# Performance work log

Measured on AMD Instinct MI355X. Metric: run time of the kernel, lower is better.

Reference implementation:

```python
import jax, jax.numpy as jnp
import numpy as np

N = 170000      # nodes
E = 2400000     # edges
F_IN = 128      # dataset.num_features
H = 64          # hidden_channels
C = 40          # dataset.num_classes
L = 8           # num_layers
ENTROPY = 1.0   # args.entropy
EPS = 1e-20


def setup_inputs() -> dict:
    key = jax.random.key(0)
    ks = jax.random.split(key, 10)
    x = jax.random.normal(ks[0], (N, F_IN), jnp.float32)
    edge_src = jax.random.randint(ks[1], (E,), 0, N)
    edge_dst = jax.random.randint(ks[2], (E,), 0, N)
    edge_weight = jax.random.uniform(ks[3], (E,), jnp.float32) / 14.0  # ~1/deg scale
    u = jax.random.uniform(ks[4], (N, L + 1), jnp.float32, 1e-6, 1.0 - 1e-6)
    gumbel = -jnp.log(-jnp.log(u))  # standard Gumbel noise for gumbel_softmax
    lin0_w = jax.random.normal(ks[5], (F_IN, H), jnp.float32) / np.float32(np.sqrt(F_IN))
    lin0_b = jnp.zeros((H,), jnp.float32)
    meta_w = jax.random.normal(ks[6], (H, 1), jnp.float32) / np.float32(np.sqrt(H))
    meta_b = jnp.zeros((1,), jnp.float32)
    lin1_w = jax.random.normal(ks[7], (H, C), jnp.float32) / np.float32(np.sqrt(H))
    lin1_b = jnp.zeros((C,), jnp.float32)
    return dict(x=x, edge_weight=edge_weight, gumbel=gumbel,
                lin0_w=lin0_w, lin0_b=lin0_b, meta_w=meta_w, meta_b=meta_b,
                lin1_w=lin1_w, lin1_b=lin1_b,
                edge_src=edge_src, edge_dst=edge_dst)


def reference(x, edge_weight, gumbel, lin0_w, lin0_b, meta_w, meta_b,
              lin1_w, lin1_b, edge_src, edge_dst):
    # input projection + relu (dropout=0 -> no-op)
    x = jnp.maximum(x @ lin0_w + lin0_b, 0.0)  # [N,H]
    xs = [x]
    # GCNII layers with conv.alpha = conv.beta = 0 -> pure edge-weighted
    # scatter-add propagation followed by relu.
    for _ in range(L):
        msg = edge_weight[:, None] * x[edge_src]              # [E,H] gather
        x = jax.ops.segment_sum(msg, edge_dst, num_segments=N)  # [N,H] scatter-add
        x = jnp.maximum(x, 0.0)
        xs.append(x)
    xMat = jnp.stack(xs, axis=1)  # [N, L+1, H] (preds == xMatrix since concat='none')
    # MetaNet: [N, L+1]
    r = jnp.squeeze(xMat @ meta_w, -1) + meta_b[0]
    # get_t: stick-breaking with sigmoid; last column uses t=1 times cumprod
    s = jax.nn.sigmoid(r)                                    # [N, L+1]
    cp_excl = jnp.concatenate(
        [jnp.ones((N, 1), s.dtype), jnp.cumprod(1.0 - s, axis=1)[:, :-1]], axis=1)
    t = s * cp_excl
    t = t.at[:, -1].set(cp_excl[:, -1])
    ent_loss = ENTROPY * (-(jnp.log(t + EPS) * t).sum(1).mean())
    # gumbel_softmax(log(t+eps), tau=1, hard=False)
    tM = jax.nn.softmax(jnp.log(t + EPS) + gumbel, axis=1)   # [N, L+1]
    # layer mixing: [N,1,L+1] @ [N,L+1,H] -> [N,H]
    out = jnp.einsum('nl,nlh->nh', tM, xMat)
    out = out @ lin1_w + lin1_b
    return jax.nn.log_softmax(out, axis=-1), ent_loss
```

## Files before the change

kernel.cpp:

```cpp
#include <hip/hip_runtime.h>
#include <hip/hip_bf16.h>

#define N_NODES 170000
#define N_EDGES 2400000
#define F_IN_   128
#define H_      64
#define C_OUT   40
#define L_LAYERS 8
#define LP1     9
#define EPS_T   1e-20f
#define ROW_ELEMS (LP1 * H_)

typedef unsigned short u16;
typedef short bf16x8 __attribute__((ext_vector_type(8)));
typedef float f32x4 __attribute__((ext_vector_type(4)));

__device__ __forceinline__ float bf2f(u16 u) {
    union { unsigned int i; float f; } c; c.i = ((unsigned int)u) << 16; return c.f;
}
__device__ __forceinline__ u16 f2bf(float f) {
    __hip_bfloat16 h = __float2bfloat16(f);
    return *reinterpret_cast<u16*>(&h);
}

__device__ __forceinline__ float waveReduceSum(float v) {
    for (int m = 32; m; m >>= 1) v += __shfl_xor(v, m, 64);
    return v;
}
__device__ __forceinline__ float waveReduceMax(float v) {
    for (int m = 32; m; m >>= 1) v = fmaxf(v, __shfl_xor(v, m, 64));
    return v;
}

__global__ __launch_bounds__(256) void k_zero4(float4* __restrict__ p) {
    p[blockIdx.x * 256 + threadIdx.x] = make_float4(0.f, 0.f, 0.f, 0.f);
}

__global__ __launch_bounds__(256) void k_hist(
    const int* __restrict__ edst, int* __restrict__ deg)
{
    int e = blockIdx.x * 256 + threadIdx.x;
    if (e < N_EDGES) atomicAdd(&deg[edst[e]], 1);
}

#define SCAN_TPB 256
#define SCAN_VPT 8
#define SCAN_EPB (SCAN_TPB * SCAN_VPT)
#define SCAN_BLOCKS ((N_NODES + SCAN_EPB - 1) / SCAN_EPB)

__global__ __launch_bounds__(SCAN_TPB) void k_scan1(
    const int* __restrict__ deg, int* __restrict__ rowstart,
    int* __restrict__ blockSums)
{
    __shared__ int tsum[SCAN_TPB];
    int tid = threadIdx.x;
    int base = blockIdx.x * SCAN_EPB + tid * SCAN_VPT;
    int vals[SCAN_VPT];
    int local = 0;
    #pragma unroll
    for (int i = 0; i < SCAN_VPT; ++i) {
        int idx = base + i;
        int v = (idx < N_NODES) ? deg[idx] : 0;
        vals[i] = local;
        local += v;
    }
    tsum[tid] = local;
    __syncthreads();
    for (int off = 1; off < SCAN_TPB; off <<= 1) {
        int v = (tid >= off) ? tsum[tid - off] : 0;
        __syncthreads();
        tsum[tid] += v;
        __syncthreads();
    }
    int texcl = tsum[tid] - local;
    #pragma unroll
    for (int i = 0; i < SCAN_VPT; ++i) {
        int idx = base + i;
        if (idx < N_NODES) rowstart[idx] = texcl + vals[i];
    }
    if (tid == SCAN_TPB - 1) blockSums[blockIdx.x] = tsum[tid];
}

__global__ __launch_bounds__(64) void k_scan2(int* __restrict__ blockSums) {
    if (threadIdx.x == 0) {
        int acc = 0;
        for (int i = 0; i < SCAN_BLOCKS; ++i) {
            int v = blockSums[i];
            blockSums[i] = acc;
            acc += v;
        }
    }
}

__global__ __launch_bounds__(SCAN_TPB) void k_scan3(
    int* __restrict__ rowstart, const int* __restrict__ blockSums)
{
    int off = blockSums[blockIdx.x];
    int base = blockIdx.x * SCAN_EPB + threadIdx.x * SCAN_VPT;
    #pragma unroll
    for (int i = 0; i < SCAN_VPT; ++i) {
        int idx = base + i;
        if (idx < N_NODES) rowstart[idx] += off;
    }
}

__global__ __launch_bounds__(256) void k_bucket(
    const int* __restrict__ esrc, const int* __restrict__ edst,
    const float* __restrict__ ew, const int* __restrict__ rowstart,
    int* __restrict__ cursor, int2* __restrict__ csr, int lo, int hi)
{
    int e = blockIdx.x * 256 + threadIdx.x;
    if (e >= N_EDGES) return;
    int d = edst[e];
    if (d < lo || d >= hi) return;
    int p = rowstart[d] + atomicAdd(&cursor[d], 1);
    csr[p] = make_int2(esrc[e], __float_as_int(ew[e]));
}

__global__ __launch_bounds__(256) void k_lin0(
    const float* __restrict__ x, const float* __restrict__ W0,
    const float* __restrict__ b0, const float* __restrict__ mw,
    const float* __restrict__ mb, u16* __restrict__ xMatB,
    float* __restrict__ r)
{
    __shared__ u16 Wt[H_ * F_IN_];
    int tid = threadIdx.x;
    for (int i = tid; i < F_IN_ * H_; i += 256) {
        int k = i >> 6, c = i & 63;
        Wt[c * F_IN_ + (k ^ ((c & 7) << 3))] = f2bf(W0[i]);
    }
    __syncthreads();

    int wave = tid >> 6, lane = tid & 63;
    int lg = lane >> 4;
    int lr = lane & 15;

    bf16x8 bfrag[4][4];
    float b0v[4], mwv[4];
    #pragma unroll
    for (int ct = 0; ct < 4; ++ct) {
        int c = ct * 16 + lr;
        #pragma unroll
        for (int kt = 0; kt < 4; ++kt) {
            int kidx = (kt * 32 + lg * 8) ^ ((c & 7) << 3);
            bfrag[ct][kt] = *reinterpret_cast<bf16x8*>(&Wt[c * F_IN_ + kidx]);
        }
        b0v[ct] = b0[c];
        mwv[ct] = mw[c];
    }
    float mb0 = mb[0];

    int nbase = blockIdx.x * 256 + wave * 64;
    #pragma unroll
    for (int m = 0; m < 4; ++m) {
        int arow = nbase + m * 16 + lr;
        int arowc = (arow < N_NODES) ? arow : (N_NODES - 1);
        const float4* xrow = (const float4*)(x + (size_t)arowc * F_IN_);
        f32x4 acc[4];
        #pragma unroll
        for (int ct = 0; ct < 4; ++ct) {
            acc[ct][0] = b0v[ct]; acc[ct][1] = b0v[ct];
            acc[ct][2] = b0v[ct]; acc[ct][3] = b0v[ct];
        }
        #pragma unroll
        for (int kt = 0; kt < 4; ++kt) {
            int k8 = kt * 8 + lg * 2;
            float4 xa = xrow[k8];
            float4 xb = xrow[k8 + 1];
            bf16x8 a;
            a[0] = (short)f2bf(xa.x); a[1] = (short)f2bf(xa.y);
            a[2] = (short)f2bf(xa.z); a[3] = (short)f2bf(xa.w);
            a[4] = (short)f2bf(xb.x); a[5] = (short)f2bf(xb.y);
            a[6] = (short)f2bf(xb.z); a[7] = (short)f2bf(xb.w);
            #pragma unroll
            for (int ct = 0; ct < 4; ++ct)
                acc[ct] = __builtin_amdgcn_mfma_f32_16x16x32_bf16(
                    a, bfrag[ct][kt], acc[ct], 0, 0, 0);
        }
        float p[4];
        #pragma unroll
        for (int reg = 0; reg < 4; ++reg) {
            int n = nbase + m * 16 + lg * 4 + reg;
            float pr = 0.f;
            #pragma unroll
            for (int ct = 0; ct < 4; ++ct) {
                float v = fmaxf(acc[ct][reg], 0.f);
                if (n < N_NODES)
                    xMatB[(size_t)n * ROW_ELEMS + ct * 16 + lr] = f2bf(v);
                pr = fmaf(v, mwv[ct], pr);
            }
            p[reg] = pr;
        }
        #pragma unroll
        for (int reg = 0; reg < 4; ++reg) {
            p[reg] += __shfl_xor(p[reg], 1, 64);
            p[reg] += __shfl_xor(p[reg], 2, 64);
            p[reg] += __shfl_xor(p[reg], 4, 64);
            p[reg] += __shfl_xor(p[reg], 8, 64);
        }
        if (lr < 4) {
            int n = nbase + m * 16 + lg * 4 + lr;
            if (n < N_NODES) r[n * LP1] = p[lr] + mb0;
        }
    }
}

__global__ __launch_bounds__(256) void k_prop(
    const u16* __restrict__ xMatB, int l,
    const int* __restrict__ rowstart, const int* __restrict__ deg,
    const int2* __restrict__ csr,
    const float* __restrict__ mw, const float* __restrict__ mb,
    u16* __restrict__ xMatOut, float* __restrict__ r)
{
    int tid = threadIdx.x, wave = tid >> 6, lane = tid & 63;
    int n = blockIdx.x * 4 + wave;
    int sl = lane & 15, q = lane >> 4;
    int start = rowstart[n];
    int d = deg[n];
    int dm1 = (d > 0) ? (d - 1) : 0;

    int myS = 0; float myW = 0.f;
    if (lane < d) {
        int2 e = csr[start + lane];
        myS = e.x; myW = __int_as_float(e.y);
    }
    const unsigned loff = (unsigned)l * H_ + sl * 4;

    float a0x = 0.f, a0y = 0.f, a0z = 0.f, a0w = 0.f;
    float a1x = 0.f, a1y = 0.f, a1z = 0.f, a1w = 0.f;
    float a2x = 0.f, a2y = 0.f, a2z = 0.f, a2w = 0.f;
    float a3x = 0.f, a3y = 0.f, a3z = 0.f, a3w = 0.f;

    int dmax = (d < 64) ? d : 64;
    int kb = 0;
    do {
        int idx0 = kb + q;
        int idx1 = kb + q + 4;
        int idx2 = kb + q + 8;
        int idx3 = kb + q + 12;
        int ic0 = (idx0 < dm1) ? idx0 : dm1;
        int ic1 = (idx1 < dm1) ? idx1 : dm1;
        int ic2 = (idx2 < dm1) ? idx2 : dm1;
        int ic3 = (idx3 < dm1) ? idx3 : dm1;
        int   s0 = __shfl(myS, ic0, 64); float w0 = __shfl(myW, ic0, 64);
        int   s1 = __shfl(myS, ic1, 64); float w1 = __shfl(myW, ic1, 64);
        int   s2 = __shfl(myS, ic2, 64); float w2 = __shfl(myW, ic2, 64);
        int   s3 = __shfl(myS, ic3, 64); float w3 = __shfl(myW, ic3, 64);
        if (idx0 >= d) w0 = 0.f;
        if (idx1 >= d) w1 = 0.f;
        if (idx2 >= d) w2 = 0.f;
        if (idx3 >= d) w3 = 0.f;
        ushort4 v0 = *reinterpret_cast<const ushort4*>(
            &xMatB[(size_t)(unsigned)s0 * ROW_ELEMS + loff]);
        ushort4 v1 = *reinterpret_cast<const ushort4*>(
            &xMatB[(size_t)(unsigned)s1 * ROW_ELEMS + loff]);
        ushort4 v2 = *reinterpret_cast<const ushort4*>(
            &xMatB[(size_t)(unsigned)s2 * ROW_ELEMS + loff]);
        ushort4 v3 = *reinterpret_cast<const ushort4*>(
            &xMatB[(size_t)(unsigned)s3 * ROW_ELEMS + loff]);
        a0x = fmaf(bf2f(v0.x), w0, a0x); a0y = fmaf(bf2f(v0.y), w0, a0y);
        a0z = fmaf(bf2f(v0.z), w0, a0z); a0w = fmaf(bf2f(v0.w), w0, a0w);
        a1x = fmaf(bf2f(v1.x), w1, a1x); a1y = fmaf(bf2f(v1.y), w1, a1y);
        a1z = fmaf(bf2f(v1.z), w1, a1z); a1w = fmaf(bf2f(v1.w), w1, a1w);
        a2x = fmaf(bf2f(v2.x), w2, a2x); a2y = fmaf(bf2f(v2.y), w2, a2y);
        a2z = fmaf(bf2f(v2.z), w2, a2z); a2w = fmaf(bf2f(v2.w), w2, a2w);
        a3x = fmaf(bf2f(v3.x), w3, a3x); a3y = fmaf(bf2f(v3.y), w3, a3y);
        a3z = fmaf(bf2f(v3.z), w3, a3z); a3w = fmaf(bf2f(v3.w), w3, a3w);
        kb += 16;
    } while (kb < dmax);

    for (int kb2 = 64; kb2 < d; kb2 += 16) {
        #pragma unroll
        for (int j = 0; j < 4; ++j) {
            int idx = kb2 + j * 4 + q;
            if (idx < d) {
                int2 e = csr[start + idx];
                float w = __int_as_float(e.y);
                ushort4 v = *reinterpret_cast<const ushort4*>(
                    &xMatB[(size_t)(unsigned)e.x * ROW_ELEMS + loff]);
                a0x = fmaf(bf2f(v.x), w, a0x);
                a0y = fmaf(bf2f(v.y), w, a0y);
                a0z = fmaf(bf2f(v.z), w, a0z);
                a0w = fmaf(bf2f(v.w), w, a0w);
            }
        }
    }

    float r0 = a0x + a1x + a2x + a3x;
    float r1 = a0y + a1y + a2y + a3y;
    float r2 = a0z + a1z + a2z + a3z;
    float r3 = a0w + a1w + a2w + a3w;
    r0 += __shfl_xor(r0, 16, 64); r0 += __shfl_xor(r0, 32, 64);
    r1 += __shfl_xor(r1, 16, 64); r1 += __shfl_xor(r1, 32, 64);
    r2 += __shfl_xor(r2, 16, 64); r2 += __shfl_xor(r2, 32, 64);
    r3 += __shfl_xor(r3, 16, 64); r3 += __shfl_xor(r3, 32, 64);
    r0 = fmaxf(r0, 0.f); r1 = fmaxf(r1, 0.f);
    r2 = fmaxf(r2, 0.f); r3 = fmaxf(r3, 0.f);
    if (q == 0) {
        ushort4 o; o.x = f2bf(r0); o.y = f2bf(r1); o.z = f2bf(r2); o.w = f2bf(r3);
        *reinterpret_cast<ushort4*>(
            &xMatOut[(size_t)n * ROW_ELEMS + (l + 1) * H_ + sl * 4]) = o;
    }
    float dot = r0 * mw[4 * sl] + r1 * mw[4 * sl + 1] +
                r2 * mw[4 * sl + 2] + r3 * mw[4 * sl + 3];
    dot += __shfl_xor(dot, 1, 64);
    dot += __shfl_xor(dot, 2, 64);
    dot += __shfl_xor(dot, 4, 64);
    dot += __shfl_xor(dot, 8, 64);
    if (lane == 0) r[n * LP1 + (l + 1)] = dot + mb[0];
}

__global__ __launch_bounds__(256) void k_gate(
    const float* __restrict__ r, const float* __restrict__ gum,
    float* __restrict__ tM, float* __restrict__ entPart)
{
    __shared__ float lds[4];
    int tid = threadIdx.x;
    int n = blockIdx.x * 256 + tid;
    float ent = 0.f;
    if (n < N_NODES) {
        float t[LP1], lg[LP1];
        float cp = 1.f;
        #pragma unroll
        for (int j = 0; j < LP1; ++j) {
            float rv = r[n * LP1 + j];
            float s = 1.f / (1.f + expf(-rv));
            t[j] = (j == L_LAYERS) ? cp : s * cp;
            cp *= (1.f - s);
        }
        float mx = -INFINITY;
        #pragma unroll
        for (int j = 0; j < LP1; ++j) {
            float lt = logf(t[j] + EPS_T);
            ent -= t[j] * lt;
            lg[j] = lt + gum[n * LP1 + j];
            mx = fmaxf(mx, lg[j]);
        }
        float se = 0.f;
        #pragma unroll
        for (int j = 0; j < LP1; ++j) { lg[j] = expf(lg[j] - mx); se += lg[j]; }
        float inv = 1.f / se;
        #pragma unroll
        for (int j = 0; j < LP1; ++j) tM[n * LP1 + j] = lg[j] * inv;
    }
    float s = waveReduceSum(ent);
    int wave = tid >> 6, lane = tid & 63;
    if (lane == 0) lds[wave] = s;
    __syncthreads();
    if (tid == 0) entPart[blockIdx.x] = lds[0] + lds[1] + lds[2] + lds[3];
}

__global__ __launch_bounds__(256) void k_final(
    const u16* __restrict__ xMatB, const float* __restrict__ tM,
    const float* __restrict__ W1, const float* __restrict__ b1,
    float* __restrict__ out)
{
    __shared__ float mixLds[4][H_];
    int tid = threadIdx.x, wave = tid >> 6, lane = tid & 63;
    int n = blockIdx.x * 4 + wave;
    float tm = (lane < LP1) ? tM[n * LP1 + lane] : 0.f;
    float m = 0.f;
    #pragma unroll
    for (int j = 0; j < LP1; ++j) {
        float w = __shfl(tm, j, 64);
        m = fmaf(w, bf2f(xMatB[(size_t)n * ROW_ELEMS + j * H_ + lane]), m);
    }
    mixLds[wave][lane] = m;
    __syncthreads();
    float o = -INFINITY;
    if (lane < C_OUT) {
        float a = b1[lane];
        #pragma unroll 8
        for (int h = 0; h < H_; ++h)
            a = fmaf(mixLds[wave][h], W1[h * C_OUT + lane], a);
        o = a;
    }
    float omx = waveReduceMax(o);
    float ex = (lane < C_OUT) ? expf(o - omx) : 0.f;
    float es = waveReduceSum(ex);
    if (lane < C_OUT)
        out[(size_t)n * C_OUT + lane] = o - omx - logf(es);
}

__global__ __launch_bounds__(256) void k_entreduce(
    const float* __restrict__ part, int n, float scale, float* __restrict__ out)
{
    __shared__ float lds[4];
    int tid = threadIdx.x;
    float s = 0.f;
    for (int i = tid; i < n; i += 256) s += part[i];
    s = waveReduceSum(s);
    int wave = tid >> 6, lane = tid & 63;
    if (lane == 0) lds[wave] = s;
    __syncthreads();
    if (tid == 0) out[0] = (lds[0] + lds[1] + lds[2] + lds[3]) * scale;
}

extern "C" void kernel_launch(void* const* d_in, const int* in_sizes, int n_in,
                              void* d_out, int out_size, void* d_ws, size_t ws_size,
                              hipStream_t stream)
{
    const float* x   = (const float*)d_in[0];
    const float* ew  = (const float*)d_in[1];
    const float* gum = (const float*)d_in[2];
    const float* W0  = (const float*)d_in[3];
    const float* b0  = (const float*)d_in[4];
    const float* mw  = (const float*)d_in[5];
    const float* mb  = (const float*)d_in[6];
    const float* W1  = (const float*)d_in[7];
    const float* b1  = (const float*)d_in[8];
    const int* esrc  = (const int*)d_in[9];
    const int* edst  = (const int*)d_in[10];
    float* out = (float*)d_out;

    const size_t xMatBytes = (size_t)N_NODES * ROW_ELEMS * sizeof(u16);
    const size_t rBytes    = (size_t)N_NODES * LP1 * sizeof(float);
    const size_t tMBytes   = (size_t)N_NODES * LP1 * sizeof(float);
    const size_t entBytes  = (size_t)((N_NODES + 255) / 256) * sizeof(float);
    const size_t degBytes  = (size_t)N_NODES * sizeof(int);
    const size_t curBytes  = (size_t)N_NODES * sizeof(int);
    const size_t rowBytes  = (size_t)N_NODES * sizeof(int);
    const size_t bsBytes   = 512;
    const size_t csrBytes  = (size_t)N_EDGES * sizeof(int2);
    const size_t need = xMatBytes + rBytes + tMBytes + entBytes + degBytes +
                        curBytes + rowBytes + bsBytes + csrBytes;
    if (ws_size < need) return;

    char* p = (char*)d_ws;
    u16*  xMatB    = (u16*)p;           p += xMatBytes;
    float* rbuf    = (float*)p;         p += rBytes;
    float* tMbuf   = (float*)p;         p += tMBytes;
    float* entP    = (float*)p;         p += entBytes;
    int*  deg      = (int*)p;           p += degBytes;
    int*  cursor   = (int*)p;           p += curBytes;
    int*  rowstart = (int*)p;           p += rowBytes;
    int*  blockSums= (int*)p;           p += bsBytes;
    int2* csr      = (int2*)p;

    const int nodeBlocks = N_NODES / 4;
    const int edgeBlocks = (N_EDGES + 255) / 256;
    const int gateBlocks = (N_NODES + 255) / 256;
    const int lin0Blocks = (N_NODES + 255) / 256;

    k_zero4<<<333, 256, 0, stream>>>((float4*)deg);
    k_hist<<<edgeBlocks, 256, 0, stream>>>(edst, deg);
    k_scan1<<<SCAN_BLOCKS, SCAN_TPB, 0, stream>>>(deg, rowstart, blockSums);
    k_scan2<<<1, 64, 0, stream>>>(blockSums);
    k_scan3<<<SCAN_BLOCKS, SCAN_TPB, 0, stream>>>(rowstart, blockSums);
    const int STEP = N_NODES / 8;
    for (int i = 0; i < 8; ++i)
        k_bucket<<<edgeBlocks, 256, 0, stream>>>(esrc, edst, ew, rowstart,
                                                 cursor, csr, i * STEP,
                                                 (i + 1) * STEP);

    k_lin0<<<lin0Blocks, 256, 0, stream>>>(x, W0, b0, mw, mb, xMatB, rbuf);
    for (int l = 0; l < L_LAYERS; ++l)
        k_prop<<<nodeBlocks, 256, 0, stream>>>(xMatB, l, rowstart, deg, csr,
                                               mw, mb, xMatB, rbuf);
    k_gate<<<gateBlocks, 256, 0, stream>>>(rbuf, gum, tMbuf, entP);
    k_final<<<nodeBlocks, 256, 0, stream>>>(xMatB, tMbuf, W1, b1, out);
    k_entreduce<<<1, 256, 0, stream>>>(entP, gateBlocks, 1.0f / N_NODES,
                                       out + (size_t)N_NODES * C_OUT);
}
```

Measured before the change: 872.9 us.

## Map eight lanes per node in propagation with 16-byte gathers

Restructures the propagation kernel so each node is handled by 8 lanes instead of a full wave. Each lane gathers 8 bf16 features (16 bytes) per edge and walks the edge list sequentially, two edges at a time. This removes the shuffle-based edge distribution and the cross-quarter reductions, and raises the number of nodes processed per block from 4 to 32. The cost is that the loop runs until the highest-degree node among the wave's 8 nodes is finished, so lanes on shorter rows sit idle, and each lane issues fewer independent loads in flight. Every lane also reloads its own CSR entries, which increases redundant index loads.

```diff
diff --git a/kernel.cpp b/kernel.cpp
--- a/kernel.cpp
+++ b/kernel.cpp
@@ -12,6 +12,7 @@
 #define ROW_ELEMS (LP1 * H_)
 
 typedef unsigned short u16;
+typedef unsigned short u16x8 __attribute__((ext_vector_type(8)));
 typedef short bf16x8 __attribute__((ext_vector_type(8)));
 typedef float f32x4 __attribute__((ext_vector_type(4)));
 
@@ -212,102 +213,56 @@
     const float* __restrict__ mw, const float* __restrict__ mb,
     u16* __restrict__ xMatOut, float* __restrict__ r)
 {
-    int tid = threadIdx.x, wave = tid >> 6, lane = tid & 63;
-    int n = blockIdx.x * 4 + wave;
-    int sl = lane & 15, q = lane >> 4;
-    int start = rowstart[n];
-    int d = deg[n];
-    int dm1 = (d > 0) ? (d - 1) : 0;
-
-    int myS = 0; float myW = 0.f;
-    if (lane < d) {
-        int2 e = csr[start + lane];
-        myS = e.x; myW = __int_as_float(e.y);
-    }
-    const unsigned loff = (unsigned)l * H_ + sl * 4;
-
-    float a0x = 0.f, a0y = 0.f, a0z = 0.f, a0w = 0.f;
-    float a1x = 0.f, a1y = 0.f, a1z = 0.f, a1w = 0.f;
-    float a2x = 0.f, a2y = 0.f, a2z = 0.f, a2w = 0.f;
-    float a3x = 0.f, a3y = 0.f, a3z = 0.f, a3w = 0.f;
-
-    int dmax = (d < 64) ? d : 64;
-    int kb = 0;
-    do {
-        int idx0 = kb + q;
-        int idx1 = kb + q + 4;
-        int idx2 = kb + q + 8;
-        int idx3 = kb + q + 12;
-        int ic0 = (idx0 < dm1) ? idx0 : dm1;
-        int ic1 = (idx1 < dm1) ? idx1 : dm1;
-        int ic2 = (idx2 < dm1) ? idx2 : dm1;
-        int ic3 = (idx3 < dm1) ? idx3 : dm1;
-        int   s0 = __shfl(myS, ic0, 64); float w0 = __shfl(myW, ic0, 64);
-        int   s1 = __shfl(myS, ic1, 64); float w1 = __shfl(myW, ic1, 64);
-        int   s2 = __shfl(myS, ic2, 64); float w2 = __shfl(myW, ic2, 64);
-        int   s3 = __shfl(myS, ic3, 64); float w3 = __shfl(myW, ic3, 64);
-        if (idx0 >= d) w0 = 0.f;
-        if (idx1 >= d) w1 = 0.f;
-        if (idx2 >= d) w2 = 0.f;
-        if (idx3 >= d) w3 = 0.f;
-        ushort4 v0 = *reinterpret_cast<const ushort4*>(
-            &xMatB[(size_t)(unsigned)s0 * ROW_ELEMS + loff]);
-        ushort4 v1 = *reinterpret_cast<const ushort4*>(
-            &xMatB[(size_t)(unsigned)s1 * ROW_ELEMS + loff]);
-        ushort4 v2 = *reinterpret_cast<const ushort4*>(
-            &xMatB[(size_t)(unsigned)s2 * ROW_ELEMS + loff]);
-        ushort4 v3 = *reinterpret_cast<const ushort4*>(
-            &xMatB[(size_t)(unsigned)s3 * ROW_ELEMS + loff]);
-        a0x = fmaf(bf2f(v0.x), w0, a0x); a0y = fmaf(bf2f(v0.y), w0, a0y);
-        a0z = fmaf(bf2f(v0.z), w0, a0z); a0w = fmaf(bf2f(v0.w), w0, a0w);
-        a1x = fmaf(bf2f(v1.x), w1, a1x); a1y = fmaf(bf2f(v1.y), w1, a1y);
-        a1z = fmaf(bf2f(v1.z), w1, a1z); a1w = fmaf(bf2f(v1.w), w1, a1w);
-        a2x = fmaf(bf2f(v2.x), w2, a2x); a2y = fmaf(bf2f(v2.y), w2, a2y);
-        a2z = fmaf(bf2f(v2.z), w2, a2z); a2w = fmaf(bf2f(v2.w), w2, a2w);
-        a3x = fmaf(bf2f(v3.x), w3, a3x); a3y = fmaf(bf2f(v3.y), w3, a3y);
-        a3z = fmaf(bf2f(v3.z), w3, a3z); a3w = fmaf(bf2f(v3.w), w3, a3w);
-        kb += 16;
-    } while (kb < dmax);
-
-    for (int kb2 = 64; kb2 < d; kb2 += 16) {
-        #pragma unroll
-        for (int j = 0; j < 4; ++j) {
-            int idx = kb2 + j * 4 + q;
-            if (idx < d) {
-                int2 e = csr[start + idx];
-                float w = __int_as_float(e.y);
-                ushort4 v = *reinterpret_cast<const ushort4*>(
-                    &xMatB[(size_t)(unsigned)e.x * ROW_ELEMS + loff]);
-                a0x = fmaf(bf2f(v.x), w, a0x);
-                a0y = fmaf(bf2f(v.y), w, a0y);
-                a0z = fmaf(bf2f(v.z), w, a0z);
-                a0w = fmaf(bf2f(v.w), w, a0w);
-            }
-        }
-    }
-
-    float r0 = a0x + a1x + a2x + a3x;
-    float r1 = a0y + a1y + a2y + a3y;
-    float r2 = a0z + a1z + a2z + a3z;
-    float r3 = a0w + a1w + a2w + a3w;
-    r0 += __shfl_xor(r0, 16, 64); r0 += __shfl_xor(r0, 32, 64);
-    r1 += __shfl_xor(r1, 16, 64); r1 += __shfl_xor(r1, 32, 64);
-    r2 += __shfl_xor(r2, 16, 64); r2 += __shfl_xor(r2, 32, 64);
-    r3 += __shfl_xor(r3, 16, 64); r3 += __shfl_xor(r3, 32, 64);
-    r0 = fmaxf(r0, 0.f); r1 = fmaxf(r1, 0.f);
-    r2 = fmaxf(r2, 0.f); r3 = fmaxf(r3, 0.f);
-    if (q == 0) {
-        ushort4 o; o.x = f2bf(r0); o.y = f2bf(r1); o.z = f2bf(r2); o.w = f2bf(r3);
-        *reinterpret_cast<ushort4*>(
-            &xMatOut[(size_t)n * ROW_ELEMS + (l + 1) * H_ + sl * 4]) = o;
-    }
-    float dot = r0 * mw[4 * sl] + r1 * mw[4 * sl + 1] +
-                r2 * mw[4 * sl + 2] + r3 * mw[4 * sl + 3];
+    int tid = threadIdx.x;
+    int oc = tid & 7;
+    int n = blockIdx.x * 32 + (tid >> 3);
+    bool valid = (n < N_NODES);
+    int start = valid ? rowstart[n] : 0;
+    int d     = valid ? deg[n]      : 0;
+
+    const unsigned loff = (unsigned)l * H_ + oc * 8;
+    float acc0[8] = {0.f,0.f,0.f,0.f,0.f,0.f,0.f,0.f};
+    float acc1[8] = {0.f,0.f,0.f,0.f,0.f,0.f,0.f,0.f};
+
+    int t = 0;
+    while (__any(t < d)) {
+        if (t < d) {
+            int2 e = csr[start + t];
+            float w = __int_as_float(e.y);
+            u16x8 v = *reinterpret_cast<const u16x8*>(
+                &xMatB[(size_t)(unsigned)e.x * ROW_ELEMS + loff]);
+            #pragma unroll
+            for (int j = 0; j < 8; ++j) acc0[j] = fmaf(bf2f(v[j]), w, acc0[j]);
+        }
+        if (t + 1 < d) {
+            int2 e = csr[start + t + 1];
+            float w = __int_as_float(e.y);
+            u16x8 v = *reinterpret_cast<const u16x8*>(
+                &xMatB[(size_t)(unsigned)e.x * ROW_ELEMS + loff]);
+            #pragma unroll
+            for (int j = 0; j < 8; ++j) acc1[j] = fmaf(bf2f(v[j]), w, acc1[j]);
+        }
+        t += 2;
+    }
+
+    float a[8];
+    #pragma unroll
+    for (int j = 0; j < 8; ++j) a[j] = fmaxf(acc0[j] + acc1[j], 0.f);
+
+    if (valid) {
+        u16x8 o;
+        #pragma unroll
+        for (int j = 0; j < 8; ++j) o[j] = f2bf(a[j]);
+        *reinterpret_cast<u16x8*>(
+            &xMatOut[(size_t)n * ROW_ELEMS + (l + 1) * H_ + oc * 8]) = o;
+    }
+    float dot = 0.f;
+    #pragma unroll
+    for (int j = 0; j < 8; ++j) dot = fmaf(a[j], mw[oc * 8 + j], dot);
     dot += __shfl_xor(dot, 1, 64);
     dot += __shfl_xor(dot, 2, 64);
     dot += __shfl_xor(dot, 4, 64);
-    dot += __shfl_xor(dot, 8, 64);
-    if (lane == 0) r[n * LP1 + (l + 1)] = dot + mb[0];
+    if (valid && oc == 0) r[n * LP1 + (l + 1)] = dot + mb[0];
 }
 
 __global__ __launch_bounds__(256) void k_gate(
@@ -441,6 +396,7 @@
     const int edgeBlocks = (N_EDGES + 255) / 256;
     const int gateBlocks = (N_NODES + 255) / 256;
     const int lin0Blocks = (N_NODES + 255) / 256;
+    const int propBlocks = (N_NODES + 31) / 32;
 
     k_zero4<<<333, 256, 0, stream>>>((float4*)deg);
     k_hist<<<edgeBlocks, 256, 0, stream>>>(edst, deg);
@@ -455,7 +411,7 @@
 
     k_lin0<<<lin0Blocks, 256, 0, stream>>>(x, W0, b0, mw, mb, xMatB, rbuf);
     for (int l = 0; l < L_LAYERS; ++l)
-        k_prop<<<nodeBlocks, 256, 0, stream>>>(xMatB, l, rowstart, deg, csr,
+        k_prop<<<propBlocks, 256, 0, stream>>>(xMatB, l, rowstart, deg, csr,
                                                mw, mb, xMatB, rbuf);
     k_gate<<<gateBlocks, 256, 0, stream>>>(rbuf, gum, tMbuf, entP);
     k_final<<<nodeBlocks, 256, 0, stream>>>(xMatB, tMbuf, W1, b1, out);
```

Result: no change. 885.1 us (+1.4%).
